# Performance work log

Hardware: AMD Instinct MI355X
Metric: run time of the kernel (lower is better)

## Reference

```python
import jax, jax.numpy as jnp
from jax import lax
import numpy as np

VOCAB, TAGS, EMBED, HIDDEN, BATCH, SEQ = 50000, 9, 300, 1000, 32, 200


def setup_inputs() -> dict:
    key = jax.random.key(0)
    ks = jax.random.split(key, 12)
    s_e = 1.0 / np.sqrt(HIDDEN)
    inp = {
        "x": jax.random.randint(ks[0], (SEQ, BATCH), 0, VOCAB),
        "y": jax.random.randint(ks[1], (SEQ, BATCH), 0, TAGS),
        "embed_w": jax.random.normal(ks[2], (VOCAB, EMBED), jnp.float32),
        "W_ih": jax.random.uniform(ks[3], (4 * HIDDEN, EMBED), jnp.float32, -s_e, s_e),
        "W_hh": jax.random.uniform(ks[4], (4 * HIDDEN, HIDDEN), jnp.float32, -s_e, s_e),
        "b_ih": jax.random.uniform(ks[5], (4 * HIDDEN,), jnp.float32, -s_e, s_e),
        "b_hh": jax.random.uniform(ks[6], (4 * HIDDEN,), jnp.float32, -s_e, s_e),
        "lin_w": jax.random.uniform(ks[7], (TAGS, HIDDEN), jnp.float32, -s_e, s_e),
        "lin_b": jax.random.uniform(ks[8], (TAGS,), jnp.float32, -s_e, s_e),
        "start_trans": jax.random.uniform(ks[9], (TAGS,), jnp.float32, -0.1, 0.1),
        "end_trans": jax.random.uniform(ks[10], (TAGS,), jnp.float32, -0.1, 0.1),
        "trans": jax.random.uniform(ks[11], (TAGS, TAGS), jnp.float32, -0.1, 0.1),
    }
    return inp


def _forward(x, y, embed_w, W_ih, W_hh, b_ih, b_hh, lin_w, lin_b, start_trans, end_trans, trans):
    T, B = x.shape
    H = W_hh.shape[1]
    embeds = embed_w[x]  # [T,B,E]
    # Precompute input contribution to gates: [T,B,4H]
    xg = jnp.einsum("tbe,ge->tbg", embeds, W_ih) + b_ih + b_hh

    def lstm_step(carry, xg_t):
        h, c = carry
        g = xg_t + h @ W_hh.T  # [B,4H]
        i, f, gg, o = jnp.split(g, 4, axis=-1)  # PyTorch gate order i,f,g,o
        c = jax.nn.sigmoid(f) * c + jax.nn.sigmoid(i) * jnp.tanh(gg)
        h = jax.nn.sigmoid(o) * jnp.tanh(c)
        return (h, c), h

    h0 = jnp.zeros((B, H), embeds.dtype)
    _, hs = lax.scan(lstm_step, (h0, h0), xg)  # hs: [T,B,H]

    tag_space = jnp.einsum("tbh,kh->tbk", hs, lin_w) + lin_b  # [T,B,K]
    # Faithful to original: log_softmax over dim=1 (the batch axis)
    emissions = jax.nn.log_softmax(tag_space, axis=1)

    # ---- CRF log-likelihood (pytorch-crf semantics, full mask, sum reduction) ----
    b_idx = jnp.arange(B)
    em_at_y = jnp.take_along_axis(emissions, y[:, :, None], axis=2)[:, :, 0]  # [T,B]
    numerator = (
        start_trans[y[0]]
        + em_at_y.sum(axis=0)
        + trans[y[:-1], y[1:]].sum(axis=0)
        + end_trans[y[-1]]
    )  # [B]

    alpha0 = start_trans[None, :] + emissions[0]  # [B,K]

    def crf_step(alpha, em_t):
        # alpha: [B,K] over previous tag; em_t: [B,K]
        nxt = jax.nn.logsumexp(alpha[:, :, None] + trans[None, :, :] + em_t[:, None, :], axis=1)
        return nxt, None

    alpha, _ = lax.scan(crf_step, alpha0, emissions[1:])
    log_z = jax.nn.logsumexp(alpha + end_trans[None, :], axis=1)  # [B]
    return (numerator - log_z).sum()


def reference(x, y, embed_w, W_ih, W_hh, b_ih, b_hh, lin_w, lin_b, start_trans, end_trans, trans):
    return _forward(x, y, embed_w, W_ih, W_hh, b_ih, b_hh, lin_w, lin_b, start_trans, end_trans, trans)
```

## Files before the change

kernel.cpp:

```cpp
#include <hip/hip_runtime.h>

#define T_SEQ 200
#define NB    32
#define NE    300
#define NH    1000
#define NK    9
#define NJ    4096
#define EPD   320
#define WSCALE 256.0f
#define HSCALE 16.0f
#define LSCALE 512.0f
#define GSCALE (1.0f / (256.0f * 16.0f))
#define TSCALE (1.0f / (16.0f * 512.0f))

typedef __attribute__((ext_vector_type(4))) float f32x4;
typedef __attribute__((ext_vector_type(8))) short s16x8;
typedef __attribute__((ext_vector_type(4))) short s16x4;
typedef unsigned long long u64;

__device__ __forceinline__ unsigned short f2bf(float f) {
    union { float f; unsigned u; } v; v.f = f;
    unsigned r = v.u + 0x7FFFu + ((v.u >> 16) & 1u);
    return (unsigned short)(r >> 16);
}
__device__ __forceinline__ float bf2f(unsigned short h) {
    union { unsigned u; float f; } v; v.u = ((unsigned)h) << 16;
    return v.f;
}
__device__ __forceinline__ float ftanh(float x) {
    float e = __expf(fminf(2.f * x, 80.f));
    return (e - 1.f) / (e + 1.f);
}
__device__ __forceinline__ float fsig(float x) {
    return 1.f / (1.f + __expf(-x));
}
__device__ __forceinline__ unsigned nt_poll(const unsigned* p) {
    unsigned r;
    asm volatile("global_load_dword %0, %1, off nt\n\t"
                 "s_waitcnt vmcnt(0)"
                 : "=v"(r) : "v"(p) : "memory");
    return r;
}
__device__ __forceinline__ void plain_pub(unsigned* p, unsigned v) {
    __hip_atomic_store(p, v, __ATOMIC_RELAXED, __HIP_MEMORY_SCOPE_WORKGROUP);
}

__global__ __launch_bounds__(256) void prep_emb(
    const int* __restrict__ x, const float* __restrict__ embed_w,
    unsigned short* __restrict__ emb_bf, unsigned* __restrict__ ctrl)
{
    const int t = blockIdx.x, tid = threadIdx.x;
    if (blockIdx.x == 0) {
        for (int i = tid; i < 2048; i += 256)
            ctrl[i] = (i == 61) ? 0xffffffffu : 0u;
    }
    for (int idx = tid; idx < NB * EPD; idx += 256) {
        int b = idx / EPD, e = idx - b * EPD;
        float v = (e < NE) ? embed_w[(size_t)x[t * NB + b] * NE + e] : 0.f;
        emb_bf[((size_t)t * NB + b) * EPD + e] = f2bf(v);
    }
}

__global__ __launch_bounds__(256) void prep_w(
    const float* __restrict__ W_ih, const float* __restrict__ b_ih,
    const float* __restrict__ b_hh, const float* __restrict__ lin_w,
    unsigned short* __restrict__ wih_bf, float* __restrict__ biasg,
    unsigned char* __restrict__ linw_q)
{
    const int blk = blockIdx.x, tid = threadIdx.x;
    for (int idx = tid; idx < 64 * EPD; idx += 256) {
        int jr = idx / EPD, e = idx - jr * EPD;
        int jp = blk * 64 + jr;
        int wgu = jp >> 7, rr = jp & 127, g = rr >> 5, uu = rr & 31;
        int m = wgu * 32 + uu;
        float v = (m < NH && e < NE) ? W_ih[(size_t)(g * NH + m) * NE + e] : 0.f;
        wih_bf[(size_t)jp * EPD + e] = f2bf(v);
    }
    if (tid < 64) {
        int jp = blk * 64 + tid;
        int wgu = jp >> 7, rr = jp & 127, g = rr >> 5, uu = rr & 31;
        int m = wgu * 32 + uu;
        biasg[jp] = (m < NH) ? (b_ih[g * NH + m] + b_hh[g * NH + m]) : 0.f;
    }
    if (blk < 16) {
        int n = blk, k = tid * 4;
        float v0 = (n < NK && k + 0 < NH) ? lin_w[(size_t)n * NH + k + 0] * LSCALE : 0.f;
        float v1 = (n < NK && k + 1 < NH) ? lin_w[(size_t)n * NH + k + 1] * LSCALE : 0.f;
        float v2 = (n < NK && k + 2 < NH) ? lin_w[(size_t)n * NH + k + 2] * LSCALE : 0.f;
        float v3 = (n < NK && k + 3 < NH) ? lin_w[(size_t)n * NH + k + 3] * LSCALE : 0.f;
        int p01 = __builtin_amdgcn_cvt_pk_fp8_f32(v0, v1, 0, false);
        int p23 = __builtin_amdgcn_cvt_pk_fp8_f32(v2, v3, 0, false);
        ((unsigned*)linw_q)[n * 256 + tid] =
            ((unsigned)p01 & 0xffffu) | ((unsigned)p23 << 16);
    }
}

__device__ __forceinline__ int gate_xg(unsigned* done, int ready, int tn, int lane) {
    while (ready <= tn) {
        unsigned v = 64u;
        if (lane < 8 && ready + lane < T_SEQ)
            v = __hip_atomic_load(&done[ready + lane], __ATOMIC_RELAXED,
                                  __HIP_MEMORY_SCOPE_AGENT);
        unsigned m = (unsigned)__ballot((int)(v >= 64u)) & 255u;
        if (m & 1u) {
            unsigned run = (m == 255u) ? 8u : (unsigned)__builtin_ctz(~m);
            ready += (int)run;
        } else {
            __builtin_amdgcn_s_sleep(1);
        }
    }
    return ready;
}

__global__ __launch_bounds__(256, 1) void lstm_kernel(
    const float* __restrict__ W_hh,
    const unsigned short* __restrict__ emb_bf,
    const unsigned short* __restrict__ wih_bf,
    const float* __restrict__ biasg,
    unsigned short* __restrict__ xg,
    unsigned char* __restrict__ h_q,
    unsigned* __restrict__ ctrl)
{
    __shared__ __align__(16) unsigned char s_w[128 * 1024];
    __shared__ int s_chunk, s_pid, s_mode;

    const int tid = threadIdx.x;

    if (tid == 0) {
        unsigned xcc;
        asm volatile("s_getreg_b32 %0, hwreg(HW_REG_XCC_ID)" : "=s"(xcc));
        xcc &= 15u;
        unsigned myidx = __hip_atomic_fetch_add(&ctrl[40 + xcc], 1u,
                             __ATOMIC_RELAXED, __HIP_MEMORY_SCOPE_AGENT);
        __threadfence();
        unsigned tot = __hip_atomic_fetch_add(&ctrl[60], 1u,
                             __ATOMIC_RELAXED, __HIP_MEMORY_SCOPE_AGENT);
        if (tot == 255u) {
            __threadfence();
            unsigned win = 0u;
            for (unsigned xx = 0; xx < 16; ++xx) {
                unsigned cx = __hip_atomic_load(&ctrl[40 + xx], __ATOMIC_RELAXED,
                                                __HIP_MEMORY_SCOPE_AGENT);
                if (cx >= 32u) { win = xx; break; }
            }
            __hip_atomic_store(&ctrl[61], win, __ATOMIC_RELAXED,
                               __HIP_MEMORY_SCOPE_AGENT);
        }
        unsigned win;
        do {
            win = __hip_atomic_load(&ctrl[61], __ATOMIC_RELAXED,
                                    __HIP_MEMORY_SCOPE_AGENT);
        } while (win == 0xffffffffu);
        bool cons = (win == xcc && myidx < 32u);
        s_chunk = cons ? (int)myidx : -1;
        s_pid = cons ? -1
                     : (int)__hip_atomic_fetch_add(&ctrl[62], 1u,
                           __ATOMIC_RELAXED, __HIP_MEMORY_SCOPE_AGENT);
    }
    __syncthreads();
    const int chunk = s_chunk;
    const int w = tid >> 6, lane = tid & 63;
    const int col = lane & 15, quad = lane >> 4;
    unsigned* slowf = ctrl;
    unsigned* fastf = ctrl + 64;
    unsigned* done  = ctrl + 256;

    if (chunk < 0) {
        const int pid = s_pid;
        for (int g = pid; g < T_SEQ * 64; g += 224) {
            const int t = g >> 6, jt = g & 63;
            const unsigned short* eb = emb_bf + (size_t)t * NB * EPD;
            const unsigned short* wb = wih_bf + (size_t)(jt * 64 + w * 16 + col) * EPD;
            const unsigned short* ea0 = eb + (size_t)col * EPD;
            const unsigned short* ea1 = eb + (size_t)(16 + col) * EPD;

            f32x4 acc0 = {0.f, 0.f, 0.f, 0.f};
            f32x4 acc1 = {0.f, 0.f, 0.f, 0.f};
#pragma unroll
            for (int kc = 0; kc < EPD / 32; ++kc) {
                int ko = kc * 32 + quad * 8;
                s16x8 a0 = *(const s16x8*)&ea0[ko];
                s16x8 a1 = *(const s16x8*)&ea1[ko];
                s16x8 bb = *(const s16x8*)&wb[ko];
                acc0 = __builtin_amdgcn_mfma_f32_16x16x32_bf16(a0, bb, acc0, 0, 0, 0);
                acc1 = __builtin_amdgcn_mfma_f32_16x16x32_bf16(a1, bb, acc1, 0, 0, 0);
            }
            const int jp = jt * 64 + w * 16 + col;
            const float bi = biasg[jp];
            size_t base = ((size_t)t * NJ + jp) * NB;
            union { s16x4 v; u64 q; } p0, p1;
#pragma unroll
            for (int r = 0; r < 4; ++r) {
                p0.v[r] = (short)f2bf(acc0[r] + bi);
                p1.v[r] = (short)f2bf(acc1[r] + bi);
            }
            __hip_atomic_store((u64*)&xg[base + quad * 4], p0.q,
                               __ATOMIC_RELAXED, __HIP_MEMORY_SCOPE_AGENT);
            __hip_atomic_store((u64*)&xg[base + 16 + quad * 4], p1.q,
                               __ATOMIC_RELAXED, __HIP_MEMORY_SCOPE_AGENT);
            __syncthreads();
            if (tid == 0)
                __hip_atomic_fetch_add(&done[t], 1u, __ATOMIC_RELAXED,
                                       __HIP_MEMORY_SCOPE_AGENT);
        }
        return;
    }

    const int bh = w >> 1, p = w & 1;
    unsigned* s_w32 = (unsigned*)s_w;

    for (int idx = tid; idx < 128 * 256; idx += 256) {
        int r = idx >> 8, dw = idx & 255;
        int g = r >> 5, uu = r & 31, m = chunk * 32 + uu;
        float4 w4 = make_float4(0.f, 0.f, 0.f, 0.f);
        if (m < NH && dw < 250)
            w4 = *(const float4*)&W_hh[(size_t)(g * NH + m) * NH + dw * 4];
        int p0 = __builtin_amdgcn_cvt_pk_fp8_f32(w4.x * WSCALE, w4.y * WSCALE, 0, false);
        int p1 = __builtin_amdgcn_cvt_pk_fp8_f32(w4.z * WSCALE, w4.w * WSCALE, 0, false);
        unsigned v = ((unsigned)p0 & 0xffffu) | ((unsigned)p1 << 16);
        int kb = dw >> 1;
        int kbs = kb ^ (r & 15);
        s_w32[r * 256 + (kbs << 1) + (dw & 1)] = v;
    }
    *(unsigned*)(h_q + (size_t)chunk * 1024 + tid * 4) = 0u;
    __syncthreads();
    if (tid == 0) {
        plain_pub(&fastf[chunk], 1u);
        __hip_atomic_store(&slowf[chunk], 1u, __ATOMIC_RELAXED,
                           __HIP_MEMORY_SCOPE_AGENT);
    }
    if (chunk == 0) {
        if (tid < 64) {
            int mode = 2;
            for (int it = 0; it < 8192; ++it) {
                unsigned v = (lane < 32) ? nt_poll(&fastf[lane]) : 1u;
                if (__all((int)(v >= 1u))) { mode = 1; break; }
            }
            if (tid == 0) {
                __hip_atomic_store(&ctrl[63], (unsigned)mode, __ATOMIC_RELAXED,
                                   __HIP_MEMORY_SCOPE_AGENT);
                s_mode = mode;
            }
        }
    } else {
        if (tid == 0) {
            unsigned m;
            do {
                m = __hip_atomic_load(&ctrl[63], __ATOMIC_RELAXED,
                                      __HIP_MEMORY_SCOPE_AGENT);
            } while (m == 0u);
            s_mode = (int)m;
        }
    }
    __syncthreads();
    const int mode = s_mode;

    int ready = 0;
    ready = gate_xg(done, ready, 0, lane);
    s16x4 xcur[4], xnxt[4];
#pragma unroll
    for (int g = 0; g < 4; ++g)
        xcur[g] = *(const s16x4*)&xg[((size_t)0 * NJ + chunk * 128 + (2 * g + p) * 16 + col) * NB
                                     + bh * 16 + quad * 4];

    float c[4] = {0.f, 0.f, 0.f, 0.f};
    const int rw = quad * 4;
    const int boff = (bh * 16 + col) * 32 + quad * 8;

    for (int t = 0; t < T_SEQ; ++t) {
        const unsigned need = (unsigned)(t + 1);
        if (mode == 1) {
            for (;;) {
                unsigned v = (lane < 32) ? nt_poll(&fastf[lane]) : need;
                if (__all((int)(v >= need))) break;
            }
        } else {
            for (;;) {
                unsigned v = (lane < 32)
                    ? __hip_atomic_load(&slowf[lane], __ATOMIC_RELAXED,
                                        __HIP_MEMORY_SCOPE_AGENT)
                    : need;
                if (__all((int)(v >= need))) break;
            }
        }
        asm volatile("" ::: "memory");

        const unsigned char* pb = h_q + (size_t)t * 32768 + boff;
        u64 a[32];
#pragma unroll
        for (int kc = 0; kc < 32; ++kc)
            a[kc] = *(const u64*)(pb + (size_t)kc * 1024);

        if (t + 1 < T_SEQ) {
            ready = gate_xg(done, ready, t + 1, lane);
#pragma unroll
            for (int g = 0; g < 4; ++g)
                xnxt[g] = *(const s16x4*)&xg[((size_t)(t + 1) * NJ + chunk * 128 + (2 * g + p) * 16 + col) * NB
                                             + bh * 16 + quad * 4];
        }

        f32x4 acc0 = {0.f, 0.f, 0.f, 0.f};
        f32x4 acc1 = {0.f, 0.f, 0.f, 0.f};
        f32x4 acc2 = {0.f, 0.f, 0.f, 0.f};
        f32x4 acc3 = {0.f, 0.f, 0.f, 0.f};
#pragma unroll
        for (int kc = 0; kc < 32; ++kc) {
            int kb = kc * 4 + quad;
            u64 b0 = *(const u64*)&s_w[((0 * 2 + p) * 16 + col) * 1024 + ((kb ^ col) << 3)];
            u64 b1 = *(const u64*)&s_w[((1 * 2 + p) * 16 + col) * 1024 + ((kb ^ col) << 3)];
            u64 b2 = *(const u64*)&s_w[((2 * 2 + p) * 16 + col) * 1024 + ((kb ^ col) << 3)];
            u64 b3 = *(const u64*)&s_w[((3 * 2 + p) * 16 + col) * 1024 + ((kb ^ col) << 3)];
            acc0 = __builtin_amdgcn_mfma_f32_16x16x32_fp8_fp8((long)a[kc], (long)b0, acc0, 0, 0, 0);
            acc1 = __builtin_amdgcn_mfma_f32_16x16x32_fp8_fp8((long)a[kc], (long)b1, acc1, 0, 0, 0);
            acc2 = __builtin_amdgcn_mfma_f32_16x16x32_fp8_fp8((long)a[kc], (long)b2, acc2, 0, 0, 0);
            acc3 = __builtin_amdgcn_mfma_f32_16x16x32_fp8_fp8((long)a[kc], (long)b3, acc3, 0, 0, 0);
        }

        float hv[4];
#pragma unroll
        for (int r = 0; r < 4; ++r) {
            float gi = acc0[r] * GSCALE + bf2f((unsigned short)xcur[0][r]);
            float gf = acc1[r] * GSCALE + bf2f((unsigned short)xcur[1][r]);
            float gg = acc2[r] * GSCALE + bf2f((unsigned short)xcur[2][r]);
            float go = acc3[r] * GSCALE + bf2f((unsigned short)xcur[3][r]);
            c[r] = fsig(gf) * c[r] + fsig(gi) * ftanh(gg);
            hv[r] = fsig(go) * ftanh(c[r]);
        }
        {
            int p01 = __builtin_amdgcn_cvt_pk_fp8_f32(hv[0] * HSCALE, hv[1] * HSCALE, 0, false);
            int p23 = __builtin_amdgcn_cvt_pk_fp8_f32(hv[2] * HSCALE, hv[3] * HSCALE, 0, false);
            unsigned char* pg = h_q + (size_t)(t + 1) * 32768 + (size_t)chunk * 1024
                              + p * 16 + col;
            pg[(bh * 16 + rw + 0) * 32] = (unsigned char)(p01 & 0xff);
            pg[(bh * 16 + rw + 1) * 32] = (unsigned char)((p01 >> 8) & 0xff);
            pg[(bh * 16 + rw + 2) * 32] = (unsigned char)(p23 & 0xff);
            pg[(bh * 16 + rw + 3) * 32] = (unsigned char)((p23 >> 8) & 0xff);
        }
        __syncthreads();
        if (tid == 0) {
            plain_pub(&fastf[chunk], (unsigned)(t + 2));
            if (mode == 2)
                __hip_atomic_store(&slowf[chunk], (unsigned)(t + 2),
                                   __ATOMIC_RELAXED, __HIP_MEMORY_SCOPE_AGENT);
        }
#pragma unroll
        for (int g = 0; g < 4; ++g) xcur[g] = xnxt[g];
    }
}

__global__ __launch_bounds__(64) void tag_gemm(
    const unsigned char* __restrict__ h_q,
    const unsigned char* __restrict__ linw_q, float* __restrict__ ts)
{
    const int m0 = blockIdx.x * 16, lane = threadIdx.x;
    const int col = lane & 15, quad = lane >> 4;
    const int m = m0 + col, t = m >> 5, b = m & 31;
    const unsigned char* pa = h_q + (size_t)(t + 1) * 32768 + b * 32 + quad * 8;
    const unsigned char* pw = linw_q + (size_t)col * 1024 + quad * 8;

    f32x4 acc = {0.f, 0.f, 0.f, 0.f};
#pragma unroll 8
    for (int kc = 0; kc < 32; ++kc) {
        u64 a  = *(const u64*)(pa + (size_t)kc * 1024);
        u64 bv = *(const u64*)(pw + kc * 32);
        acc = __builtin_amdgcn_mfma_f32_16x16x32_fp8_fp8((long)a, (long)bv, acc, 0, 0, 0);
    }
#pragma unroll
    for (int r = 0; r < 4; ++r)
        ts[(size_t)(m0 + quad * 4 + r) * 16 + col] = acc[r] * TSCALE;
}

__global__ __launch_bounds__(320) void em_kernel(
    const float* __restrict__ ts, const float* __restrict__ lin_b,
    float* __restrict__ em)
{
    __shared__ float s_ts[NB * NK];
    __shared__ float s_lse[NK];
    const int t = blockIdx.x, tid = threadIdx.x;
    float val = 0.f;
    int b = tid / NK, k = tid - b * NK;
    if (tid < NB * NK) {
        val = ts[(size_t)(t * NB + b) * 16 + k] + lin_b[k];
        s_ts[b * NK + k] = val;
    }
    __syncthreads();
    if (tid < NK) {
        float m = -1e30f;
        for (int bb = 0; bb < NB; ++bb) m = fmaxf(m, s_ts[bb * NK + tid]);
        float s = 0.f;
        for (int bb = 0; bb < NB; ++bb) s += __expf(s_ts[bb * NK + tid] - m);
        s_lse[tid] = m + __logf(s);
    }
    __syncthreads();
    if (tid < NB * NK)
        em[((size_t)t * NB + b) * NK + k] = val - s_lse[k];
}

__global__ __launch_bounds__(320) void crf_kernel(
    const int* __restrict__ y, const float* __restrict__ em,
    const float* __restrict__ start_trans, const float* __restrict__ end_trans,
    const float* __restrict__ trans, float* __restrict__ out)
{
    __shared__ float s_trans[NK * NK];
    __shared__ float s_alpha[NB * NK];
    __shared__ float s_red[NB];
    const int tid = threadIdx.x;
    if (tid < NK * NK) s_trans[tid] = trans[tid];
    __syncthreads();

    float num = 0.f;
    if (tid < NB) {
        int b = tid, yp = y[b];
        num = start_trans[yp] + em[(size_t)b * NK + yp];
        for (int t = 1; t < T_SEQ; ++t) {
            int yc = y[t * NB + b];
            num += s_trans[yp * NK + yc] + em[((size_t)t * NB + b) * NK + yc];
            yp = yc;
        }
        num += end_trans[yp];
    }

    const int b = tid / NK, k = tid - (tid / NK) * NK;
    if (tid < NB * NK)
        s_alpha[tid] = start_trans[k] + em[(size_t)b * NK + k];
    __syncthreads();

    for (int t = 1; t < T_SEQ; ++t) {
        float nv = 0.f;
        if (tid < NB * NK) {
            float m = -1e30f;
#pragma unroll
            for (int i = 0; i < NK; ++i)
                m = fmaxf(m, s_alpha[b * NK + i] + s_trans[i * NK + k]);
            float s = 0.f;
#pragma unroll
            for (int i = 0; i < NK; ++i)
                s += __expf(s_alpha[b * NK + i] + s_trans[i * NK + k] - m);
            nv = em[((size_t)t * NB + b) * NK + k] + m + __logf(s);
        }
        __syncthreads();
        if (tid < NB * NK) s_alpha[tid] = nv;
        __syncthreads();
    }

    if (tid < NB) {
        float m = -1e30f;
        for (int k2 = 0; k2 < NK; ++k2)
            m = fmaxf(m, s_alpha[tid * NK + k2] + end_trans[k2]);
        float s = 0.f;
        for (int k2 = 0; k2 < NK; ++k2)
            s += __expf(s_alpha[tid * NK + k2] + end_trans[k2] - m);
        s_red[tid] = num - (m + __logf(s));
    }
    __syncthreads();
    if (tid == 0) {
        float tot = 0.f;
        for (int i = 0; i < NB; ++i) tot += s_red[i];
        out[0] = tot;
    }
}

extern "C" void kernel_launch(void* const* d_in, const int* in_sizes, int n_in,
                              void* d_out, int out_size, void* d_ws, size_t ws_size,
                              hipStream_t stream)
{
    const int*   x           = (const int*)d_in[0];
    const int*   y           = (const int*)d_in[1];
    const float* embed_w     = (const float*)d_in[2];
    const float* W_ih        = (const float*)d_in[3];
    const float* W_hh        = (const float*)d_in[4];
    const float* b_ih        = (const float*)d_in[5];
    const float* b_hh        = (const float*)d_in[6];
    const float* lin_w       = (const float*)d_in[7];
    const float* lin_b       = (const float*)d_in[8];
    const float* start_trans = (const float*)d_in[9];
    const float* end_trans   = (const float*)d_in[10];
    const float* trans       = (const float*)d_in[11];
    float* out = (float*)d_out;

    char* ws = (char*)d_ws;
    unsigned short* xg     = (unsigned short*)(ws);
    float*          ts     = (float*)(ws);
    unsigned char*  h_q    = (unsigned char*)(ws + 52428800);
    unsigned char*  linw_q = (unsigned char*)(ws + 59015168);
    float*          em     = (float*)(ws + 65601536);
    unsigned*       ctrl   = (unsigned*)(ws + 65831936);
    float*          biasg  = (float*)(ws + 65840128);
    unsigned short* emb_bf = (unsigned short*)(ws + 65856512);
    unsigned short* wih_bf = (unsigned short*)(ws + 69952512);

    prep_emb<<<dim3(T_SEQ), 256, 0, stream>>>(x, embed_w, emb_bf, ctrl);
    prep_w<<<dim3(64), 256, 0, stream>>>(W_ih, b_ih, b_hh, lin_w, wih_bf, biasg, linw_q);

    lstm_kernel<<<dim3(256), 256, 0, stream>>>(W_hh, emb_bf, wih_bf, biasg,
                                               xg, h_q, ctrl);

    tag_gemm<<<dim3(400), 64, 0, stream>>>(h_q, linw_q, ts);
    em_kernel<<<dim3(T_SEQ), 320, 0, stream>>>(ts, lin_b, em);
    crf_kernel<<<dim3(1), 320, 0, stream>>>(y, em, start_trans, end_trans, trans, out);
}
```

Measured before the change: 1.136 ms.

## Split LSTM recurrence into two independent batch-half groups on separate XCDs

The persistent recurrent kernel now splits the batch into two halves of 16, each run by its own group of 32 blocks on a different XCC. Each group has its own flag arrays and its own h_q region, so the cross-block barrier for every step only spans blocks on one XCC and the per-step h load is halved. Only two waves per block do the recurrence, and the other two just match the barriers. Fewer blocks are left for the input-gate GEMM producers, and each recurrent block now holds the full W_hh slice while doing half the MFMA work, so matrix throughput per step is lower.

```diff
diff --git a/kernel.cpp b/kernel.cpp
--- a/kernel.cpp
+++ b/kernel.cpp
@@ -122,7 +122,7 @@
     unsigned* __restrict__ ctrl)
 {
     __shared__ __align__(16) unsigned char s_w[128 * 1024];
-    __shared__ int s_chunk, s_pid, s_mode;
+    __shared__ int s_chunk, s_grp, s_pid, s_mode;
 
     const int tid = threadIdx.x;
 
@@ -137,13 +137,16 @@
                              __ATOMIC_RELAXED, __HIP_MEMORY_SCOPE_AGENT);
         if (tot == 255u) {
             __threadfence();
-            unsigned win = 0u;
+            unsigned w0 = 0xffu, w1 = 0xffu;
             for (unsigned xx = 0; xx < 16; ++xx) {
                 unsigned cx = __hip_atomic_load(&ctrl[40 + xx], __ATOMIC_RELAXED,
                                                 __HIP_MEMORY_SCOPE_AGENT);
-                if (cx >= 32u) { win = xx; break; }
-            }
-            __hip_atomic_store(&ctrl[61], win, __ATOMIC_RELAXED,
+                if (cx >= 32u) {
+                    if (w0 == 0xffu) w0 = xx;
+                    else { w1 = xx; break; }
+                }
+            }
+            __hip_atomic_store(&ctrl[61], w0 | (w1 << 8), __ATOMIC_RELAXED,
                                __HIP_MEMORY_SCOPE_AGENT);
         }
         unsigned win;
@@ -151,9 +154,13 @@
             win = __hip_atomic_load(&ctrl[61], __ATOMIC_RELAXED,
                                     __HIP_MEMORY_SCOPE_AGENT);
         } while (win == 0xffffffffu);
-        bool cons = (win == xcc && myidx < 32u);
-        s_chunk = cons ? (int)myidx : -1;
-        s_pid = cons ? -1
+        unsigned w0 = win & 0xffu, w1 = (win >> 8) & 0xffu;
+        int grp = -1;
+        if (xcc == w0 && myidx < 32u) grp = 0;
+        else if (xcc == w1 && myidx < 32u) grp = 1;
+        s_grp = grp;
+        s_chunk = (grp >= 0) ? (int)myidx : -1;
+        s_pid = (grp >= 0) ? -1
                      : (int)__hip_atomic_fetch_add(&ctrl[62], 1u,
                            __ATOMIC_RELAXED, __HIP_MEMORY_SCOPE_AGENT);
     }
@@ -161,13 +168,11 @@
     const int chunk = s_chunk;
     const int w = tid >> 6, lane = tid & 63;
     const int col = lane & 15, quad = lane >> 4;
-    unsigned* slowf = ctrl;
-    unsigned* fastf = ctrl + 64;
-    unsigned* done  = ctrl + 256;
+    unsigned* done = ctrl + 256;
 
     if (chunk < 0) {
         const int pid = s_pid;
-        for (int g = pid; g < T_SEQ * 64; g += 224) {
+        for (int g = pid; g < T_SEQ * 64; g += 192) {
             const int t = g >> 6, jt = g & 63;
             const unsigned short* eb = emb_bf + (size_t)t * NB * EPD;
             const unsigned short* wb = wih_bf + (size_t)(jt * 64 + w * 16 + col) * EPD;
@@ -206,7 +211,10 @@
         return;
     }
 
-    const int bh = w >> 1, p = w & 1;
+    const int grp = s_grp;
+    const size_t GOFF = (size_t)grp * 16384;
+    unsigned* fastf = ctrl + 64 + grp * 64;
+    unsigned* slowf = ctrl + grp * 96;
     unsigned* s_w32 = (unsigned*)s_w;
 
     for (int idx = tid; idx < 128 * 256; idx += 256) {
@@ -222,14 +230,15 @@
         int kbs = kb ^ (r & 15);
         s_w32[r * 256 + (kbs << 1) + (dw & 1)] = v;
     }
-    *(unsigned*)(h_q + (size_t)chunk * 1024 + tid * 4) = 0u;
+    if (tid < 128)
+        *(unsigned*)(h_q + GOFF + (size_t)chunk * 512 + tid * 4) = 0u;
     __syncthreads();
     if (tid == 0) {
         plain_pub(&fastf[chunk], 1u);
         __hip_atomic_store(&slowf[chunk], 1u, __ATOMIC_RELAXED,
                            __HIP_MEMORY_SCOPE_AGENT);
     }
-    if (chunk == 0) {
+    if (grp == 0 && chunk == 0) {
         if (tid < 64) {
             int mode = 2;
             for (int it = 0; it < 8192; ++it) {
@@ -255,17 +264,23 @@
     __syncthreads();
     const int mode = s_mode;
 
+    if (w >= 2) {
+        for (int t = 0; t < T_SEQ; ++t) __syncthreads();
+        return;
+    }
+    const int p = w;
+
     int ready = 0;
     ready = gate_xg(done, ready, 0, lane);
     s16x4 xcur[4], xnxt[4];
 #pragma unroll
     for (int g = 0; g < 4; ++g)
         xcur[g] = *(const s16x4*)&xg[((size_t)0 * NJ + chunk * 128 + (2 * g + p) * 16 + col) * NB
-                                     + bh * 16 + quad * 4];
+                                     + grp * 16 + quad * 4];
 
     float c[4] = {0.f, 0.f, 0.f, 0.f};
     const int rw = quad * 4;
-    const int boff = (bh * 16 + col) * 32 + quad * 8;
+    const int boff = col * 32 + quad * 8;
 
     for (int t = 0; t < T_SEQ; ++t) {
         const unsigned need = (unsigned)(t + 1);
@@ -285,18 +300,18 @@
         }
         asm volatile("" ::: "memory");
 
-        const unsigned char* pb = h_q + (size_t)t * 32768 + boff;
+        const unsigned char* pb = h_q + (size_t)t * 32768 + GOFF + boff;
         u64 a[32];
 #pragma unroll
         for (int kc = 0; kc < 32; ++kc)
-            a[kc] = *(const u64*)(pb + (size_t)kc * 1024);
+            a[kc] = *(const u64*)(pb + (size_t)kc * 512);
 
         if (t + 1 < T_SEQ) {
             ready = gate_xg(done, ready, t + 1, lane);
 #pragma unroll
             for (int g = 0; g < 4; ++g)
                 xnxt[g] = *(const s16x4*)&xg[((size_t)(t + 1) * NJ + chunk * 128 + (2 * g + p) * 16 + col) * NB
-                                             + bh * 16 + quad * 4];
+                                             + grp * 16 + quad * 4];
         }
 
         f32x4 acc0 = {0.f, 0.f, 0.f, 0.f};
@@ -329,12 +344,12 @@
         {
             int p01 = __builtin_amdgcn_cvt_pk_fp8_f32(hv[0] * HSCALE, hv[1] * HSCALE, 0, false);
             int p23 = __builtin_amdgcn_cvt_pk_fp8_f32(hv[2] * HSCALE, hv[3] * HSCALE, 0, false);
-            unsigned char* pg = h_q + (size_t)(t + 1) * 32768 + (size_t)chunk * 1024
+            unsigned char* pg = h_q + (size_t)(t + 1) * 32768 + GOFF + (size_t)chunk * 512
                               + p * 16 + col;
-            pg[(bh * 16 + rw + 0) * 32] = (unsigned char)(p01 & 0xff);
-            pg[(bh * 16 + rw + 1) * 32] = (unsigned char)((p01 >> 8) & 0xff);
-            pg[(bh * 16 + rw + 2) * 32] = (unsigned char)(p23 & 0xff);
-            pg[(bh * 16 + rw + 3) * 32] = (unsigned char)((p23 >> 8) & 0xff);
+            pg[(rw + 0) * 32] = (unsigned char)(p01 & 0xff);
+            pg[(rw + 1) * 32] = (unsigned char)((p01 >> 8) & 0xff);
+            pg[(rw + 2) * 32] = (unsigned char)(p23 & 0xff);
+            pg[(rw + 3) * 32] = (unsigned char)((p23 >> 8) & 0xff);
         }
         __syncthreads();
         if (tid == 0) {
@@ -355,13 +370,15 @@
     const int m0 = blockIdx.x * 16, lane = threadIdx.x;
     const int col = lane & 15, quad = lane >> 4;
     const int m = m0 + col, t = m >> 5, b = m & 31;
-    const unsigned char* pa = h_q + (size_t)(t + 1) * 32768 + b * 32 + quad * 8;
+    const int g = b >> 4, bl = b & 15;
+    const unsigned char* pa = h_q + (size_t)(t + 1) * 32768 + (size_t)g * 16384
+                            + bl * 32 + quad * 8;
     const unsigned char* pw = linw_q + (size_t)col * 1024 + quad * 8;
 
     f32x4 acc = {0.f, 0.f, 0.f, 0.f};
 #pragma unroll 8
     for (int kc = 0; kc < 32; ++kc) {
-        u64 a  = *(const u64*)(pa + (size_t)kc * 1024);
+        u64 a  = *(const u64*)(pa + (size_t)kc * 512);
         u64 bv = *(const u64*)(pw + kc * 32);
         acc = __builtin_amdgcn_mfma_f32_16x16x32_fp8_fp8((long)a, (long)bv, acc, 0, 0, 0);
     }
```

New measurement: 1.040 ms. 1.09x faster.
